# Kernel optimization log

Hardware: AMD Instinct MI355X
Metric: run time of the kernel (lower is better)

Reference implementation:

```python
import jax, jax.numpy as jnp
import numpy as np

N, E, F_IN, F_OUT, K = 10000, 640000, 256, 64, 4


def setup_inputs() -> dict:
    key = jax.random.key(0)
    ks = jax.random.split(key, 8)
    feat = jax.random.normal(ks[0], (N, F_IN), dtype=jnp.float32)
    feat_a = jax.random.normal(ks[1], (N, F_IN), dtype=jnp.float32)
    edge_index = jax.random.randint(ks[2], (2, E), 0, N)
    graph_neigh = jax.random.uniform(ks[3], (N, N), dtype=jnp.float32)
    W = jax.random.normal(ks[4], ((K + 1) * F_IN, F_OUT), dtype=jnp.float32) * 0.05
    Wb = jax.random.normal(ks[5], (F_OUT, F_OUT), dtype=jnp.float32) * 0.05
    b = jnp.zeros((), dtype=jnp.float32)
    return {"feat": feat, "feat_a": feat_a, "edge_index": edge_index,
            "graph_neigh": graph_neigh, "W": W, "Wb": Wb, "b": b}


def _sym_norm(edge_index, num_nodes):
    # add_remaining_self_loops with all-ones weights: drop existing self-loops,
    # append a weight-1 self loop per node (fill_value=1, improved=False)
    row, col = edge_index[0], edge_index[1]
    w = jnp.where(row == col, 0.0, 1.0).astype(jnp.float32)
    loop = jnp.arange(num_nodes)
    row = jnp.concatenate([row, loop])
    col = jnp.concatenate([col, loop])
    w = jnp.concatenate([w, jnp.ones((num_nodes,), jnp.float32)])
    deg = jax.ops.segment_sum(w, row, num_segments=num_nodes)
    dis = jnp.where(deg > 0, jax.lax.rsqrt(deg), 0.0)  # inf -> 0
    norm = dis[row] * w * dis[col]
    return row, col, norm


def _comb_unweighted(x, row, col, norm, k_hops):
    # K-hop propagation: out[dst] += norm * x[src]; concat hops 0..K
    xs = [x]
    for _ in range(k_hops):
        msg = norm[:, None] * xs[-1][row]          # gather + scale  [E', F]
        xs.append(jax.ops.segment_sum(msg, col, num_segments=x.shape[0]))
    return jnp.concatenate(xs, axis=1)             # [N, F*(K+1)]


def _avg_readout(emb, mask):
    vsum = mask @ emb                              # [N, F_OUT]
    row_sum = jnp.sum(mask, axis=1, keepdims=True)
    g = vsum / row_sum
    nrm = jnp.linalg.norm(g, axis=1, keepdims=True)
    return g / jnp.maximum(nrm, 1e-12)             # F.normalize p=2


def _disc(c, h_pl, h_mi, Wb, b):
    # nn.Bilinear(n_h, n_h, 1): sc = h^T Wb c + b, per node
    sc1 = jnp.einsum('nd,de,ne->n', h_pl, Wb, c) + b
    sc2 = jnp.einsum('nd,de,ne->n', h_mi, Wb, c) + b
    return jnp.stack([sc1, sc2], axis=1)           # [N, 2]


def reference(feat, feat_a, edge_index, graph_neigh, W, Wb, b):
    row, col, norm = _sym_norm(edge_index, feat.shape[0])
    h = _comb_unweighted(feat, row, col, norm, K) @ W
    h_a = _comb_unweighted(feat_a, row, col, norm, K) @ W
    emb = jax.nn.relu(h)
    emb_a = jax.nn.relu(h_a)
    g = jax.nn.sigmoid(_avg_readout(emb, graph_neigh))
    g_a = jax.nn.sigmoid(_avg_readout(emb_a, graph_neigh))
    ret = _disc(g, emb, emb_a, Wb, b)
    ret_a = _disc(g_a, emb_a, emb, Wb, b)
    return emb, ret, ret_a
```

## Files before the change

### kernel.cpp

```cpp
#include <hip/hip_runtime.h>
#include <hip/hip_bf16.h>
#include <hip/hip_fp16.h>

typedef float f32x4 __attribute__((ext_vector_type(4)));
typedef short s16x8 __attribute__((ext_vector_type(8)));
typedef unsigned int u32x4 __attribute__((ext_vector_type(4)));

#define F_IN 256
#define F_OUT 64
#define KSPLIT 9
#define HBLK 120

static __device__ __forceinline__ short f2bf(float f){
  union { float f; unsigned u; } x; x.f = f;
  unsigned r = (x.u + 0x7FFFu + ((x.u >> 16) & 1u)) >> 16;
  return (short)r;
}

static __device__ __forceinline__ unsigned pack_rtne(float f0, float f1){
  return ((unsigned)(unsigned short)f2bf(f0)) | ((unsigned)(unsigned short)f2bf(f1) << 16);
}

static __device__ __forceinline__ unsigned pack_trunc(float f0, float f1){
  return (__float_as_uint(f0) >> 16) | (__float_as_uint(f1) & 0xFFFF0000u);
}

static __device__ __forceinline__ float bf_lo(unsigned u){ return __uint_as_float(u << 16); }
static __device__ __forceinline__ float bf_hi(unsigned u){ return __uint_as_float(u & 0xFFFF0000u); }
static __device__ __forceinline__ float h16(unsigned u){
  return __half2float(__ushort_as_half((unsigned short)(u >> 16)));
}

union FragU { u32x4 u; s16x8 s; };


__global__ void wt_zero_kernel(const float* __restrict__ W, short* __restrict__ WT,
                               int* __restrict__ deg, int* __restrict__ counts, int n){
  int idx = blockIdx.x * blockDim.x + threadIdx.x;
  if (idx < n){ deg[idx] = 0; counts[idx] = 0; }
  if (idx < 5 * 64 * 256){
    int k = idx & 255, c = (idx >> 8) & 63, by = idx >> 14;
    WT[idx] = f2bf(W[(size_t)(by * 256 + k) * 64 + c]);
  }
}


__global__ __launch_bounds__(1024) void hist_kernel(const int* __restrict__ ei, int E,
                                                    int* __restrict__ deg,
                                                    int* __restrict__ counts,
                                                    int* __restrict__ blkcnt, int n){
  __shared__ unsigned bins[10240];
  int tid = threadIdx.x;
  int per = (E + HBLK - 1) / HBLK;
  int e0 = blockIdx.x * per, e1 = min(E, e0 + per);

  for (int i = tid; i < n; i += 1024) bins[i] = 0u;
  __syncthreads();
  for (int e = e0 + tid; e < e1; e += 1024){
    int r = ei[e], c = ei[E + e];
    if (r != c){
      atomicAdd(&bins[c], 1u);
      atomicAdd(&bins[r], 0x10000u);
    }
  }
  __syncthreads();
  for (int i = tid; i < n; i += 1024){
    unsigned v = bins[i];
    int cc = (int)(v & 0xFFFFu), rc = (int)(v >> 16);
    blkcnt[(size_t)blockIdx.x * n + i] = cc;
    if (cc) atomicAdd(&counts[i], cc);
    if (rc) atomicAdd(&deg[i], rc);
  }
}


__global__ __launch_bounds__(1024) void scan_kernel(const int* __restrict__ counts,
                                                    const int* __restrict__ deg,
                                                    float* __restrict__ dis,
                                                    float* __restrict__ selfnorm,
                                                    int* __restrict__ offsets, int n){
  const int C = 10;
  __shared__ int vals[10240];
  __shared__ int wsums[16];
  int tid = threadIdx.x, wid = tid >> 6, lane = tid & 63;
  for (int i = tid; i < 10240; i += 1024) vals[i] = (i < n) ? counts[i] : 0;
  for (int i = tid; i < n; i += 1024){
    float d = (float)(deg[i] + 1);
    dis[i] = rsqrtf(d);
    selfnorm[i] = 1.0f / d;
  }
  __syncthreads();
  int base = tid * C;
  int s = 0;
  #pragma unroll
  for (int i = 0; i < C; ++i) s += vals[base + i];
  int x = s;
  #pragma unroll
  for (int off = 1; off < 64; off <<= 1){
    int y = __shfl_up(x, off);
    if (lane >= off) x += y;
  }
  if (lane == 63) wsums[wid] = x;
  __syncthreads();
  if (wid == 0){
    int v = (lane < 16) ? wsums[lane] : 0;
    int xx = v;
    #pragma unroll
    for (int off = 1; off < 16; off <<= 1){
      int y = __shfl_up(xx, off);
      if (lane >= off) xx += y;
    }
    if (lane < 16) wsums[lane] = xx - v;
  }
  __syncthreads();
  int run = (x - s) + wsums[wid];
  if (tid == 1023) offsets[n] = run + s;
  #pragma unroll
  for (int i = 0; i < C; ++i){ int v = vals[base + i]; vals[base + i] = run; run += v; }
  __syncthreads();
  for (int i = tid; i < 10240; i += 1024)
    if (i < n) offsets[i] = vals[i];
}


__global__ void blkbase_kernel(const int* __restrict__ offsets, const int* __restrict__ blkcnt,
                               int* __restrict__ blkbase, int n){
  int bin = blockIdx.x * blockDim.x + threadIdx.x;
  if (bin >= n) return;
  int run = offsets[bin];
  #pragma unroll 8
  for (int blk = 0; blk < HBLK; ++blk){
    blkbase[(size_t)blk * n + bin] = run;
    run += blkcnt[(size_t)blk * n + bin];
  }
}


__global__ __launch_bounds__(1024) void fill_kernel(const int* __restrict__ ei, int E,
                                                    const float* __restrict__ dis,
                                                    const int* __restrict__ blkbase,
                                                    unsigned* __restrict__ csr, int n){
  __shared__ int bins[10240];
  int tid = threadIdx.x;
  int per = (E + HBLK - 1) / HBLK;
  int e0 = blockIdx.x * per, e1 = min(E, e0 + per);
  for (int i = tid; i < n; i += 1024) bins[i] = blkbase[(size_t)blockIdx.x * n + i];
  __syncthreads();
  for (int e = e0 + tid; e < e1; e += 1024){
    int r = ei[e], c = ei[E + e];
    if (r == c) continue;
    int pos = atomicAdd(&bins[c], 1);
    unsigned h = (unsigned)__half_as_ushort(__float2half(dis[r] * dis[c]));
    csr[pos] = (unsigned)r | (h << 16);
  }
}


__global__ __launch_bounds__(64) void fgemm_kernel(const float* __restrict__ X0,
                                                   const float* __restrict__ X1,
                                                   const short* __restrict__ WT,
                                                   float* __restrict__ Yc0,
                                                   unsigned* __restrict__ YcB,
                                                   short* __restrict__ t0bf, int M){
  int bz = blockIdx.y;
  const float* X = bz ? X1 : X0;
  int l = threadIdx.x, lr = l & 15, g = l >> 4;
  int row0 = blockIdx.x * 16;
  const f32x4* ap = (const f32x4*)(X + (size_t)(row0 + lr) * F_IN + g * 8);
  s16x8 afr[8];
  #pragma unroll
  for (int it = 0; it < 8; ++it){
    f32x4 x0 = ap[it * 8], x1 = ap[it * 8 + 1];
    FragU af;
    af.u[0] = pack_rtne(x0[0], x0[1]); af.u[1] = pack_rtne(x0[2], x0[3]);
    af.u[2] = pack_rtne(x1[0], x1[1]); af.u[3] = pack_rtne(x1[2], x1[3]);
    afr[it] = af.s;
  }
  for (int by = 0; by < 5; ++by){
    f32x4 acc[4];
    #pragma unroll
    for (int ct = 0; ct < 4; ++ct) acc[ct] = (f32x4){0,0,0,0};
    const s16x8* bp[4];
    #pragma unroll
    for (int ct = 0; ct < 4; ++ct)
      bp[ct] = (const s16x8*)(WT + ((size_t)by * 64 + ct * 16 + lr) * F_IN + g * 8);
    #pragma unroll
    for (int it = 0; it < 8; ++it)
      #pragma unroll
      for (int ct = 0; ct < 4; ++ct)
        acc[ct] = __builtin_amdgcn_mfma_f32_16x16x32_bf16(afr[it], bp[ct][it * 4], acc[ct], 0, 0, 0);
    if (by == 0){
      float* yp = Yc0 + (size_t)bz * 64;
      #pragma unroll
      for (int ct = 0; ct < 4; ++ct)
        #pragma unroll
        for (int i = 0; i < 4; ++i)
          yp[(size_t)(row0 + g * 4 + i) * 128 + ct * 16 + lr] = acc[ct][i];
    } else if (by <= 3){
      unsigned* yb = YcB + (size_t)(by - 1) * (M >> 1) * 128 + (size_t)bz * 64;
      #pragma unroll
      for (int ct = 0; ct < 4; ++ct)
        #pragma unroll
        for (int i = 0; i < 4; i += 2){
          int grow = row0 + g * 4 + i;
          yb[(size_t)(grow >> 1) * 128 + ct * 16 + lr] = pack_rtne(acc[ct][i], acc[ct][i + 1]);
        }
    } else {
      short* tb = t0bf + (size_t)bz * 64;
      #pragma unroll
      for (int ct = 0; ct < 4; ++ct)
        #pragma unroll
        for (int i = 0; i < 4; ++i)
          tb[(size_t)(row0 + g * 4 + i) * 128 + ct * 16 + lr] = f2bf(acc[ct][i]);
    }
  }
}


__global__ __launch_bounds__(256) void gather_kernel(const void* __restrict__ Yk,
    const unsigned* __restrict__ tinb, const int* __restrict__ offsets,
    const unsigned* __restrict__ csr, const float* __restrict__ selfnorm,
    unsigned* __restrict__ toutb, float* __restrict__ toutf, int n, int wantf, int ykbf){
  int wid = threadIdx.x >> 6, lane = threadIdx.x & 63;
  int node = blockIdx.x * 4 + wid;
  if (node >= n) return;
  int e0 = offsets[node], e1 = offsets[node + 1];
  float sn = selfnorm[node];
  unsigned t0 = tinb[(size_t)node * 64 + lane];
  float ykx, yky;
  if (ykbf){
    const unsigned* yp = (const unsigned*)Yk + (size_t)(node >> 1) * 128 + lane * 2;
    unsigned u0 = yp[0], u1 = yp[1];
    if (node & 1){ ykx = bf_hi(u0); yky = bf_hi(u1); }
    else         { ykx = bf_lo(u0); yky = bf_lo(u1); }
  } else {
    float2 yk = ((const float2*)Yk)[(size_t)node * 64 + lane];
    ykx = yk.x; yky = yk.y;
  }
  float ax = ykx + sn * bf_lo(t0);
  float ay = yky + sn * bf_hi(t0);
  int i = e0;
  for (; i + 8 <= e1; i += 8){
    unsigned q0 = csr[i],   q1 = csr[i+1], q2 = csr[i+2], q3 = csr[i+3];
    unsigned q4 = csr[i+4], q5 = csr[i+5], q6 = csr[i+6], q7 = csr[i+7];
    unsigned v0 = tinb[(size_t)(q0 & 0xFFFFu) * 64 + lane];
    unsigned v1 = tinb[(size_t)(q1 & 0xFFFFu) * 64 + lane];
    unsigned v2 = tinb[(size_t)(q2 & 0xFFFFu) * 64 + lane];
    unsigned v3 = tinb[(size_t)(q3 & 0xFFFFu) * 64 + lane];
    unsigned v4 = tinb[(size_t)(q4 & 0xFFFFu) * 64 + lane];
    unsigned v5 = tinb[(size_t)(q5 & 0xFFFFu) * 64 + lane];
    unsigned v6 = tinb[(size_t)(q6 & 0xFFFFu) * 64 + lane];
    unsigned v7 = tinb[(size_t)(q7 & 0xFFFFu) * 64 + lane];
    float w0 = h16(q0), w1 = h16(q1), w2 = h16(q2), w3 = h16(q3);
    float w4 = h16(q4), w5 = h16(q5), w6 = h16(q6), w7 = h16(q7);
    ax += w0 * bf_lo(v0); ay += w0 * bf_hi(v0);
    ax += w1 * bf_lo(v1); ay += w1 * bf_hi(v1);
    ax += w2 * bf_lo(v2); ay += w2 * bf_hi(v2);
    ax += w3 * bf_lo(v3); ay += w3 * bf_hi(v3);
    ax += w4 * bf_lo(v4); ay += w4 * bf_hi(v4);
    ax += w5 * bf_lo(v5); ay += w5 * bf_hi(v5);
    ax += w6 * bf_lo(v6); ay += w6 * bf_hi(v6);
    ax += w7 * bf_lo(v7); ay += w7 * bf_hi(v7);
  }
  for (; i + 4 <= e1; i += 4){
    unsigned q0 = csr[i], q1 = csr[i+1], q2 = csr[i+2], q3 = csr[i+3];
    unsigned v0 = tinb[(size_t)(q0 & 0xFFFFu) * 64 + lane];
    unsigned v1 = tinb[(size_t)(q1 & 0xFFFFu) * 64 + lane];
    unsigned v2 = tinb[(size_t)(q2 & 0xFFFFu) * 64 + lane];
    unsigned v3 = tinb[(size_t)(q3 & 0xFFFFu) * 64 + lane];
    float w0 = h16(q0), w1 = h16(q1), w2 = h16(q2), w3 = h16(q3);
    ax += w0 * bf_lo(v0); ay += w0 * bf_hi(v0);
    ax += w1 * bf_lo(v1); ay += w1 * bf_hi(v1);
    ax += w2 * bf_lo(v2); ay += w2 * bf_hi(v2);
    ax += w3 * bf_lo(v3); ay += w3 * bf_hi(v3);
  }
  for (; i < e1; ++i){
    unsigned q = csr[i];
    float w = h16(q);
    unsigned v = tinb[(size_t)(q & 0xFFFFu) * 64 + lane];
    ax += w * bf_lo(v); ay += w * bf_hi(v);
  }
  if (wantf){
    float2 r; r.x = ax; r.y = ay;
    ((float2*)toutf)[(size_t)node * 64 + lane] = r;
  } else {
    toutb[(size_t)node * 64 + lane] = pack_rtne(ax, ay);
  }
}


__global__ __launch_bounds__(256) void relu_trans_kernel(const float* __restrict__ u,
    float* __restrict__ emb, float* __restrict__ emb_a, short* __restrict__ embBT, int n){
  __shared__ short lds[128 * 72];
  int t = threadIdx.x;
  int node0 = blockIdx.x * 64;
  int nl = t >> 2;
  int f0 = (t & 3) * 32;
  int node = node0 + nl;
  if (node < n){
    const f32x4* up = (const f32x4*)(u + (size_t)node * 128 + f0);
    float* dst = (f0 < 64) ? (emb + (size_t)node * 64 + f0)
                           : (emb_a + (size_t)node * 64 + (f0 - 64));
    #pragma unroll
    for (int j4 = 0; j4 < 8; ++j4){
      f32x4 v = up[j4];
      #pragma unroll
      for (int e = 0; e < 4; ++e){
        float x = v[e] > 0.0f ? v[e] : 0.0f;
        v[e] = x;
        lds[(f0 + j4 * 4 + e) * 72 + nl] = f2bf(x);
      }
      ((f32x4*)dst)[j4] = v;
    }
  }
  __syncthreads();
  int f = t >> 1, c0 = (t & 1) * 32;
  short* op = embBT + (size_t)f * n + node0 + c0;
  const short* lp = lds + f * 72 + c0;
  if (node0 + 64 <= n){
    #pragma unroll
    for (int j = 0; j < 4; ++j)
      *(s16x8*)(op + j * 8) = *(const s16x8*)(lp + j * 8);
  } else {
    for (int j = 0; j < 32; ++j)
      if (node0 + c0 + j < n) op[j] = lp[j];
  }
}


__global__ __launch_bounds__(256, 3) void readout_kernel(const float* __restrict__ mask,
    const short* __restrict__ embBT, unsigned* __restrict__ vsumP, int n){
  __shared__ float Ab[2][128][32];
  __shared__ short Bb[2][128][32];
  int t = threadIdx.x;
  int w = t >> 6, l = t & 63, lr = l & 15, g = l >> 4;
  int row0 = blockIdx.x * 128;
  int ks = blockIdx.y;

  int steps_total = (n + 31) >> 5;
  int per = steps_total / KSPLIT, rem = steps_total % KSPLIT;
  int sbeg = ks * per + (ks < rem ? ks : rem);
  int scnt = per + (ks < rem ? 1 : 0);
  bool tail = ((sbeg + scnt) == steps_total) && ((n & 31) != 0);
  int nf = scnt - (tail ? 1 : 0);
  int kb0 = sbeg << 5;

  int aswz = ((l & 7) ^ ((l >> 3) & 7)) << 2;
  const float* asrc[4];
  #pragma unroll
  for (int j = 0; j < 4; ++j){
    int ar = row0 + w * 32 + j * 8 + (l >> 3);
    asrc[j] = mask + (size_t)min(ar, n - 1) * n + aswz;
  }
  int bcol = w * 32 + (l >> 2);
  int bswz = ((l & 3) ^ ((l >> 3) & 3)) << 3;
  const short* bsrc0 = embBT + (size_t)bcol * n + bswz;
  const short* bsrc1 = embBT + (size_t)(bcol + 16) * n + bswz;

  #define GLDS(gp, lp) __builtin_amdgcn_global_load_lds( \
      (const __attribute__((address_space(1))) void*)(const void*)(gp), \
      (__attribute__((address_space(3))) void*)(void*)(lp), 16, 0, 0)
  #define STAGE(kb, bi) do{ \
    GLDS(asrc[0] + (kb), &Ab[bi][w * 32     ][0]); \
    GLDS(asrc[1] + (kb), &Ab[bi][w * 32 +  8][0]); \
    GLDS(asrc[2] + (kb), &Ab[bi][w * 32 + 16][0]); \
    GLDS(asrc[3] + (kb), &Ab[bi][w * 32 + 24][0]); \
    GLDS(bsrc0 + (kb), &Bb[bi][w * 32     ][0]); \
    GLDS(bsrc1 + (kb), &Bb[bi][w * 32 + 16][0]); \
  }while(0)

  f32x4 acc[2][8];
  #pragma unroll
  for (int rt = 0; rt < 2; ++rt)
    #pragma unroll
    for (int ct = 0; ct < 8; ++ct) acc[rt][ct] = (f32x4){0,0,0,0};

  if (nf > 0) STAGE(kb0, 0);
  if (nf > 1) STAGE(kb0 + 32, 1);

  for (int s = 0; s < nf; ++s){
    if (s + 1 < nf) asm volatile("s_waitcnt vmcnt(6)" ::: "memory");
    else            asm volatile("s_waitcnt vmcnt(0)" ::: "memory");
    __builtin_amdgcn_s_barrier();
    int cur = s & 1;
    s16x8 bfr[8];
    #pragma unroll
    for (int ct = 0; ct < 8; ++ct)
      bfr[ct] = *(const s16x8*)&Bb[cur][ct * 16 + lr][(g ^ ((lr >> 1) & 3)) << 3];
    #pragma unroll
    for (int rt = 0; rt < 2; ++rt){
      f32x4 x0 = *(const f32x4*)&Ab[cur][w * 32 + rt * 16 + lr][((2 * g)     ^ (lr & 7)) << 2];
      f32x4 x1 = *(const f32x4*)&Ab[cur][w * 32 + rt * 16 + lr][((2 * g + 1) ^ (lr & 7)) << 2];
      FragU af;
      af.u[0] = pack_trunc(x0[0], x0[1]); af.u[1] = pack_trunc(x0[2], x0[3]);
      af.u[2] = pack_trunc(x1[0], x1[1]); af.u[3] = pack_trunc(x1[2], x1[3]);
      #pragma unroll
      for (int ct = 0; ct < 8; ++ct)
        acc[rt][ct] = __builtin_amdgcn_mfma_f32_16x16x32_bf16(af.s, bfr[ct], acc[rt][ct], 0, 0, 0);
    }
    asm volatile("s_waitcnt lgkmcnt(0)" ::: "memory");
    __builtin_amdgcn_s_barrier();
    if (s + 2 < nf) STAGE(kb0 + (s + 2) * 32, cur);
  }
  #undef STAGE
  #undef GLDS

  if (tail){
    int kb = kb0 + nf * 32;
    int kleft = n - kb;
    const s16x8 bz = {0,0,0,0,0,0,0,0};
    s16x8 bfr[8];
    #pragma unroll
    for (int ct = 0; ct < 8; ++ct)
      bfr[ct] = (g * 8 < kleft) ? *(const s16x8*)(embBT + (size_t)(ct * 16 + lr) * n + kb + g * 8) : bz;
    #pragma unroll
    for (int rt = 0; rt < 2; ++rt){
      FragU af; af.u = (u32x4){0,0,0,0};
      int r = row0 + w * 32 + rt * 16 + lr;
      if (g * 8 < kleft && r < n){
        const f32x4* p = (const f32x4*)(mask + (size_t)r * n + kb + g * 8);
        f32x4 r0 = p[0], r1 = p[1];
        af.u[0] = pack_trunc(r0[0], r0[1]); af.u[1] = pack_trunc(r0[2], r0[3]);
        af.u[2] = pack_trunc(r1[0], r1[1]); af.u[3] = pack_trunc(r1[2], r1[3]);
      }
      #pragma unroll
      for (int ct = 0; ct < 8; ++ct)
        acc[rt][ct] = __builtin_amdgcn_mfma_f32_16x16x32_bf16(af.s, bfr[ct], acc[rt][ct], 0, 0, 0);
    }
  }

  unsigned* vs = vsumP + (size_t)ks * (n >> 1) * 128;
  #pragma unroll
  for (int rt = 0; rt < 2; ++rt){
    int rbase = row0 + w * 32 + rt * 16;
    #pragma unroll
    for (int ct = 0; ct < 8; ++ct)
      #pragma unroll
      for (int i = 0; i < 4; i += 2){
        int gr = rbase + g * 4 + i;
        if (gr < n)
          vs[(size_t)(gr >> 1) * 128 + ct * 16 + lr] = pack_rtne(acc[rt][ct][i], acc[rt][ct][i + 1]);
      }
  }
}


__global__ __launch_bounds__(256) void gnorm_disc_kernel(const unsigned* __restrict__ vsumP,
    const float* __restrict__ emb, const float* __restrict__ emb_a,
    const float* __restrict__ Wb, const float* __restrict__ bptr,
    float* __restrict__ ret, float* __restrict__ reta, int n){
  __shared__ float Wl[64][65];
  int t = threadIdx.x;
  for (int i = t; i < 4096; i += 256) Wl[i >> 6][i & 63] = Wb[i];
  __syncthreads();
  int wid = t >> 6, lane = t & 63;
  int node = blockIdx.x * 4 + wid;
  if (node >= n) return;

  size_t stride = (size_t)(n >> 1) * 128;
  size_t rowoff = (size_t)(node >> 1) * 128;
  bool hi = (node & 1) != 0;
  float v1 = 0.0f, v2 = 0.0f;
  #pragma unroll
  for (int ks = 0; ks < KSPLIT; ++ks){
    unsigned a = vsumP[ks * stride + rowoff + lane];
    unsigned b = vsumP[ks * stride + rowoff + 64 + lane];
    v1 += hi ? bf_hi(a) : bf_lo(a);
    v2 += hi ? bf_hi(b) : bf_lo(b);
  }
  float s1 = v1 * v1, s2 = v2 * v2;
  for (int off = 32; off >= 1; off >>= 1){
    s1 += __shfl_xor(s1, off);
    s2 += __shfl_xor(s2, off);
  }
  float i1 = v1 / fmaxf(sqrtf(s1), 1e-12f);
  float i2 = v2 / fmaxf(sqrtf(s2), 1e-12f);
  float g1 = 1.0f / (1.0f + expf(-i1));
  float g2 = 1.0f / (1.0f + expf(-i2));

  float e1 = emb[(size_t)node * 64 + lane];
  float e2 = emb_a[(size_t)node * 64 + lane];
  float u1 = 0.0f, u2 = 0.0f;
  for (int e = 0; e < 64; ++e){
    float wv = Wl[lane][e];
    u1 += wv * __shfl(g1, e);
    u2 += wv * __shfl(g2, e);
  }
  float p1 = e1 * u1, p2 = e2 * u1, p3 = e2 * u2, p4 = e1 * u2;
  for (int off = 32; off >= 1; off >>= 1){
    p1 += __shfl_xor(p1, off); p2 += __shfl_xor(p2, off);
    p3 += __shfl_xor(p3, off); p4 += __shfl_xor(p4, off);
  }
  if (lane == 0){
    float b = bptr[0];
    ret[(size_t)node * 2 + 0]  = p1 + b;
    ret[(size_t)node * 2 + 1]  = p2 + b;
    reta[(size_t)node * 2 + 0] = p3 + b;
    reta[(size_t)node * 2 + 1] = p4 + b;
  }
}


extern "C" void kernel_launch(void* const* d_in, const int* in_sizes, int n_in,
                              void* d_out, int out_size, void* d_ws, size_t ws_size,
                              hipStream_t stream) {
  const float* feat   = (const float*)d_in[0];
  const float* feat_a = (const float*)d_in[1];
  const int*   ei     = (const int*)d_in[2];
  const float* mask   = (const float*)d_in[3];
  const float* W      = (const float*)d_in[4];
  const float* Wb     = (const float*)d_in[5];
  const float* bsc    = (const float*)d_in[6];
  const int n = in_sizes[0] / F_IN;
  const int E = in_sizes[2] / 2;
  const size_t sl128 = (size_t)n * 128;

  float* out  = (float*)d_out;
  float* ret  = out + (size_t)n * F_OUT;
  float* reta = ret + (size_t)n * 2;

  char* wsb = (char*)d_ws;
  size_t off = 0;
  #define WSALLOC(ptr, T, cnt) T* ptr = (T*)(wsb + off); off = (off + sizeof(T)*(size_t)(cnt) + 255) & ~(size_t)255
  WSALLOC(deg, int, n);
  WSALLOC(counts, int, n);
  WSALLOC(offs, int, n + 1);
  WSALLOC(dis, float, n);
  WSALLOC(selfnorm, float, n);
  WSALLOC(csr, unsigned, E);
  WSALLOC(blkcnt, int, (size_t)HBLK * n);
  WSALLOC(blkbase, int, (size_t)HBLK * n);
  WSALLOC(WT, short, 5 * 64 * 256);
  WSALLOC(Yc0, float, sl128);
  WSALLOC(YcB, unsigned, (size_t)3 * (n >> 1) * 128);
  WSALLOC(t0bf, short, sl128);
  WSALLOC(tb0, unsigned, (size_t)n * 64);
  WSALLOC(tb1, unsigned, (size_t)n * 64);
  WSALLOC(u1, float, sl128);
  WSALLOC(emb_a, float, (size_t)n * F_OUT);
  WSALLOC(embBT, short, (size_t)128 * n);
  WSALLOC(vsumP, unsigned, (size_t)KSPLIT * (n >> 1) * 128);
  (void)ws_size; (void)n_in; (void)out_size;

  wt_zero_kernel<<<(5 * 64 * 256 + 255) / 256, 256, 0, stream>>>(W, WT, deg, counts, n);
  hist_kernel<<<HBLK, 1024, 0, stream>>>(ei, E, deg, counts, blkcnt, n);
  scan_kernel<<<1, 1024, 0, stream>>>(counts, deg, dis, selfnorm, offs, n);
  blkbase_kernel<<<(n + 255) / 256, 256, 0, stream>>>(offs, blkcnt, blkbase, n);
  fill_kernel<<<HBLK, 1024, 0, stream>>>(ei, E, dis, blkbase, csr, n);

  fgemm_kernel<<<dim3(n / 16, 2), 64, 0, stream>>>(feat, feat_a, WT, Yc0, YcB, t0bf, n);

  int gb = (n + 3) / 4;
  const size_t ybs = (size_t)(n >> 1) * 128;
  gather_kernel<<<gb, 256, 0, stream>>>(YcB + 2 * ybs, (unsigned*)t0bf, offs, csr, selfnorm, tb0, (float*)0, n, 0, 1);
  gather_kernel<<<gb, 256, 0, stream>>>(YcB + 1 * ybs, tb0, offs, csr, selfnorm, tb1, (float*)0, n, 0, 1);
  gather_kernel<<<gb, 256, 0, stream>>>(YcB + 0 * ybs, tb1, offs, csr, selfnorm, tb0, (float*)0, n, 0, 1);
  gather_kernel<<<gb, 256, 0, stream>>>(Yc0, tb0, offs, csr, selfnorm, (unsigned*)0, u1, n, 1, 0);
  relu_trans_kernel<<<(n + 63) / 64, 256, 0, stream>>>(u1, out, emb_a, embBT, n);

  readout_kernel<<<dim3((n + 127) / 128, KSPLIT), 256, 0, stream>>>(mask, embBT, vsumP, n);
  gnorm_disc_kernel<<<gb, 256, 0, stream>>>(vsumP, out, emb_a, Wb, bsc, ret, reta, n);
}
```

Baseline: 299.5 us.

## Replace global histogram atomics with reduction pass and split fgemm hops across warps

The histogram kernel now writes packed per-block bin counts and a new sumcnt kernel reduces them per node, replacing global atomicAdds and the zeroing of deg/counts. The feature GEMM goes from one 64-thread wave looping over five weight blocks to a 320-thread block that stages the 16-row input tile in shared memory, with each wave computing one weight block. This adds parallelism to fgemm and removes atomic contention, at the cost of an extra kernel launch and a full pass over the per-block count array.

```diff
diff --git a/kernel.cpp b/kernel.cpp
--- a/kernel.cpp
+++ b/kernel.cpp
@@ -34,10 +34,8 @@
 union FragU { u32x4 u; s16x8 s; };
 
 
-__global__ void wt_zero_kernel(const float* __restrict__ W, short* __restrict__ WT,
-                               int* __restrict__ deg, int* __restrict__ counts, int n){
+__global__ void wt_kernel(const float* __restrict__ W, short* __restrict__ WT){
   int idx = blockIdx.x * blockDim.x + threadIdx.x;
-  if (idx < n){ deg[idx] = 0; counts[idx] = 0; }
   if (idx < 5 * 64 * 256){
     int k = idx & 255, c = (idx >> 8) & 63, by = idx >> 14;
     WT[idx] = f2bf(W[(size_t)(by * 256 + k) * 64 + c]);
@@ -46,9 +44,7 @@
 
 
 __global__ __launch_bounds__(1024) void hist_kernel(const int* __restrict__ ei, int E,
-                                                    int* __restrict__ deg,
-                                                    int* __restrict__ counts,
-                                                    int* __restrict__ blkcnt, int n){
+                                                    unsigned* __restrict__ blkcntP, int n){
   __shared__ unsigned bins[10240];
   int tid = threadIdx.x;
   int per = (E + HBLK - 1) / HBLK;
@@ -64,13 +60,24 @@
     }
   }
   __syncthreads();
-  for (int i = tid; i < n; i += 1024){
-    unsigned v = bins[i];
-    int cc = (int)(v & 0xFFFFu), rc = (int)(v >> 16);
-    blkcnt[(size_t)blockIdx.x * n + i] = cc;
-    if (cc) atomicAdd(&counts[i], cc);
-    if (rc) atomicAdd(&deg[i], rc);
-  }
+  for (int i = tid; i < n; i += 1024)
+    blkcntP[(size_t)blockIdx.x * n + i] = bins[i];
+}
+
+
+__global__ void sumcnt_kernel(const unsigned* __restrict__ blkcntP,
+                              int* __restrict__ counts, int* __restrict__ deg, int n){
+  int bin = blockIdx.x * blockDim.x + threadIdx.x;
+  if (bin >= n) return;
+  int cc = 0, rc = 0;
+  #pragma unroll 8
+  for (int blk = 0; blk < HBLK; ++blk){
+    unsigned v = blkcntP[(size_t)blk * n + bin];
+    cc += (int)(v & 0xFFFFu);
+    rc += (int)(v >> 16);
+  }
+  counts[bin] = cc;
+  deg[bin] = rc;
 }
 
 
@@ -123,7 +130,7 @@
 }
 
 
-__global__ void blkbase_kernel(const int* __restrict__ offsets, const int* __restrict__ blkcnt,
+__global__ void blkbase_kernel(const int* __restrict__ offsets, const unsigned* __restrict__ blkcntP,
                                int* __restrict__ blkbase, int n){
   int bin = blockIdx.x * blockDim.x + threadIdx.x;
   if (bin >= n) return;
@@ -131,7 +138,7 @@
   #pragma unroll 8
   for (int blk = 0; blk < HBLK; ++blk){
     blkbase[(size_t)blk * n + bin] = run;
-    run += blkcnt[(size_t)blk * n + bin];
+    run += (int)(blkcntP[(size_t)blk * n + bin] & 0xFFFFu);
   }
 }
 
@@ -156,63 +163,71 @@
 }
 
 
-__global__ __launch_bounds__(64) void fgemm_kernel(const float* __restrict__ X0,
-                                                   const float* __restrict__ X1,
-                                                   const short* __restrict__ WT,
-                                                   float* __restrict__ Yc0,
-                                                   unsigned* __restrict__ YcB,
-                                                   short* __restrict__ t0bf, int M){
-  int bz = blockIdx.y;
+__global__ __launch_bounds__(320) void fgemm_kernel(const float* __restrict__ X0,
+                                                    const float* __restrict__ X1,
+                                                    const short* __restrict__ WT,
+                                                    float* __restrict__ Yc0,
+                                                    unsigned* __restrict__ YcB,
+                                                    short* __restrict__ t0bf, int M){
+  __shared__ float Xs[16][260];
+  int tid = threadIdx.x;
+  int w = tid >> 6, l = tid & 63, lr = l & 15, g = l >> 4;
+  int row0 = blockIdx.x * 16, bz = blockIdx.y;
   const float* X = bz ? X1 : X0;
-  int l = threadIdx.x, lr = l & 15, g = l >> 4;
-  int row0 = blockIdx.x * 16;
-  const f32x4* ap = (const f32x4*)(X + (size_t)(row0 + lr) * F_IN + g * 8);
+  for (int i = tid; i < 1024; i += 320){
+    int r = i >> 6, c4 = (i & 63) << 2;
+    *(f32x4*)&Xs[r][c4] = *(const f32x4*)(X + (size_t)(row0 + r) * F_IN + c4);
+  }
+  __syncthreads();
+
   s16x8 afr[8];
   #pragma unroll
   for (int it = 0; it < 8; ++it){
-    f32x4 x0 = ap[it * 8], x1 = ap[it * 8 + 1];
+    f32x4 x0 = *(const f32x4*)&Xs[lr][it * 32 + g * 8];
+    f32x4 x1 = *(const f32x4*)&Xs[lr][it * 32 + g * 8 + 4];
     FragU af;
     af.u[0] = pack_rtne(x0[0], x0[1]); af.u[1] = pack_rtne(x0[2], x0[3]);
     af.u[2] = pack_rtne(x1[0], x1[1]); af.u[3] = pack_rtne(x1[2], x1[3]);
     afr[it] = af.s;
   }
-  for (int by = 0; by < 5; ++by){
-    f32x4 acc[4];
-    #pragma unroll
-    for (int ct = 0; ct < 4; ++ct) acc[ct] = (f32x4){0,0,0,0};
-    const s16x8* bp[4];
+
+  int by = w;
+  f32x4 acc[4];
+  #pragma unroll
+  for (int ct = 0; ct < 4; ++ct) acc[ct] = (f32x4){0,0,0,0};
+  const s16x8* bp[4];
+  #pragma unroll
+  for (int ct = 0; ct < 4; ++ct)
+    bp[ct] = (const s16x8*)(WT + ((size_t)by * 64 + ct * 16 + lr) * F_IN + g * 8);
+  #pragma unroll
+  for (int it = 0; it < 8; ++it)
     #pragma unroll
     for (int ct = 0; ct < 4; ++ct)
-      bp[ct] = (const s16x8*)(WT + ((size_t)by * 64 + ct * 16 + lr) * F_IN + g * 8);
-    #pragma unroll
-    for (int it = 0; it < 8; ++it)
-      #pragma unroll
-      for (int ct = 0; ct < 4; ++ct)
-        acc[ct] = __builtin_amdgcn_mfma_f32_16x16x32_bf16(afr[it], bp[ct][it * 4], acc[ct], 0, 0, 0);
-    if (by == 0){
-      float* yp = Yc0 + (size_t)bz * 64;
-      #pragma unroll
-      for (int ct = 0; ct < 4; ++ct)
-        #pragma unroll
-        for (int i = 0; i < 4; ++i)
-          yp[(size_t)(row0 + g * 4 + i) * 128 + ct * 16 + lr] = acc[ct][i];
-    } else if (by <= 3){
-      unsigned* yb = YcB + (size_t)(by - 1) * (M >> 1) * 128 + (size_t)bz * 64;
-      #pragma unroll
-      for (int ct = 0; ct < 4; ++ct)
-        #pragma unroll
-        for (int i = 0; i < 4; i += 2){
-          int grow = row0 + g * 4 + i;
-          yb[(size_t)(grow >> 1) * 128 + ct * 16 + lr] = pack_rtne(acc[ct][i], acc[ct][i + 1]);
-        }
-    } else {
-      short* tb = t0bf + (size_t)bz * 64;
-      #pragma unroll
-      for (int ct = 0; ct < 4; ++ct)
-        #pragma unroll
-        for (int i = 0; i < 4; ++i)
-          tb[(size_t)(row0 + g * 4 + i) * 128 + ct * 16 + lr] = f2bf(acc[ct][i]);
-    }
+      acc[ct] = __builtin_amdgcn_mfma_f32_16x16x32_bf16(afr[it], bp[ct][it * 4], acc[ct], 0, 0, 0);
+
+  if (by == 0){
+    float* yp = Yc0 + (size_t)bz * 64;
+    #pragma unroll
+    for (int ct = 0; ct < 4; ++ct)
+      #pragma unroll
+      for (int i = 0; i < 4; ++i)
+        yp[(size_t)(row0 + g * 4 + i) * 128 + ct * 16 + lr] = acc[ct][i];
+  } else if (by <= 3){
+    unsigned* yb = YcB + (size_t)(by - 1) * (M >> 1) * 128 + (size_t)bz * 64;
+    #pragma unroll
+    for (int ct = 0; ct < 4; ++ct)
+      #pragma unroll
+      for (int i = 0; i < 4; i += 2){
+        int grow = row0 + g * 4 + i;
+        yb[(size_t)(grow >> 1) * 128 + ct * 16 + lr] = pack_rtne(acc[ct][i], acc[ct][i + 1]);
+      }
+  } else {
+    short* tb = t0bf + (size_t)bz * 64;
+    #pragma unroll
+    for (int ct = 0; ct < 4; ++ct)
+      #pragma unroll
+      for (int i = 0; i < 4; ++i)
+        tb[(size_t)(row0 + g * 4 + i) * 128 + ct * 16 + lr] = f2bf(acc[ct][i]);
   }
 }
 
@@ -528,7 +543,7 @@
   WSALLOC(dis, float, n);
   WSALLOC(selfnorm, float, n);
   WSALLOC(csr, unsigned, E);
-  WSALLOC(blkcnt, int, (size_t)HBLK * n);
+  WSALLOC(blkcntP, unsigned, (size_t)HBLK * n);
   WSALLOC(blkbase, int, (size_t)HBLK * n);
   WSALLOC(WT, short, 5 * 64 * 256);
   WSALLOC(Yc0, float, sl128);
@@ -542,13 +557,14 @@
   WSALLOC(vsumP, unsigned, (size_t)KSPLIT * (n >> 1) * 128);
   (void)ws_size; (void)n_in; (void)out_size;
 
-  wt_zero_kernel<<<(5 * 64 * 256 + 255) / 256, 256, 0, stream>>>(W, WT, deg, counts, n);
-  hist_kernel<<<HBLK, 1024, 0, stream>>>(ei, E, deg, counts, blkcnt, n);
+  wt_kernel<<<(5 * 64 * 256 + 255) / 256, 256, 0, stream>>>(W, WT);
+  hist_kernel<<<HBLK, 1024, 0, stream>>>(ei, E, blkcntP, n);
+  sumcnt_kernel<<<(n + 255) / 256, 256, 0, stream>>>(blkcntP, counts, deg, n);
   scan_kernel<<<1, 1024, 0, stream>>>(counts, deg, dis, selfnorm, offs, n);
-  blkbase_kernel<<<(n + 255) / 256, 256, 0, stream>>>(offs, blkcnt, blkbase, n);
+  blkbase_kernel<<<(n + 255) / 256, 256, 0, stream>>>(offs, blkcntP, blkbase, n);
   fill_kernel<<<HBLK, 1024, 0, stream>>>(ei, E, dis, blkbase, csr, n);
 
-  fgemm_kernel<<<dim3(n / 16, 2), 64, 0, stream>>>(feat, feat_a, WT, Yc0, YcB, t0bf, n);
+  fgemm_kernel<<<dim3(n / 16, 2), 320, 0, stream>>>(feat, feat_a, WT, Yc0, YcB, t0bf, n);
 
   int gb = (n + 3) / 4;
   const size_t ybs = (size_t)(n >> 1) * 128;
```

Measured after the change: 295.8 us, median of 2. No clear change (-1.2%).
